# Optimization experiments

Hardware: AMD Instinct MI355X
Metric: run time of the kernel (lower is better)

## Reference

```python
import jax, jax.numpy as jnp
import numpy as np

SCALE = 1.0  # alpha / rank = 32 / 32


def setup_inputs() -> dict:
    key = jax.random.key(0)
    k_x, k_w, k_b, k_a, k_bb = jax.random.split(key, 5)
    B, S, D = 4, 4096, 3072
    depth, rank = 4, 32
    x = jax.random.normal(k_x, (B, S, D), dtype=jnp.float32)
    W = jax.random.normal(k_w, (D, D), dtype=jnp.float32) * (1.0 / np.sqrt(D))
    b = jax.random.normal(k_b, (D,), dtype=jnp.float32) * 0.02
    lora_A = jax.random.normal(k_a, (depth, rank, D), dtype=jnp.float32) * (1.0 / np.sqrt(D))
    lora_B = jax.random.normal(k_bb, (depth, D, rank), dtype=jnp.float32) * 0.02
    return {"x": x, "W": W, "b": b, "lora_A": lora_A, "lora_B": lora_B}


def reference(x, W, b, lora_A, lora_B):
    # base: y = x @ W.T + b
    base_out = jnp.einsum('bsi,oi->bso', x, W) + b
    # stacked LoRA: sum_d (x @ A_d.T @ B_d.T); dropout=0 -> identity
    # down-project to rank per depth: [B,S,depth,rank]
    z = jnp.einsum('bsi,dri->bsdr', x, lora_A)
    lora_out = jnp.einsum('bsdr,dor->bso', z, lora_B)
    return base_out + lora_out * SCALE
```

## Files before the change

kernel.cpp:

```cpp
#include <hip/hip_runtime.h>
#include <hip/hip_bf16.h>


typedef unsigned short ushort_t;
typedef short bf16x8 __attribute__((ext_vector_type(8)));
typedef float floatx4 __attribute__((ext_vector_type(4)));
typedef unsigned short ushortx4 __attribute__((ext_vector_type(4)));

__device__ __forceinline__ ushort_t f2bf(float f) {
    __hip_bfloat16 h = __float2bfloat16(f);
    return *(ushort_t*)&h;
}

__device__ __forceinline__ void async_load16(const void* g, void* l) {
    __builtin_amdgcn_global_load_lds(
        (const __attribute__((address_space(1))) void*)g,
        (__attribute__((address_space(3))) void*)l,
        16, 0, 0);
}

__global__ __launch_bounds__(256)
void cvt_kernel(const float* __restrict__ in, ushort_t* __restrict__ out, int n4) {
    int i = blockIdx.x * 256 + threadIdx.x;
    if (i < n4) {
        const float4 v = ((const float4*)in)[i];
        ushortx4 o = { f2bf(v.x), f2bf(v.y), f2bf(v.z), f2bf(v.w) };
        ((ushortx4*)out)[i] = o;
    }
}

__global__ __launch_bounds__(256)
void transpose_loraB_kernel(const float* __restrict__ lb,
                            ushort_t* __restrict__ out) {
    int idx = blockIdx.x * 256 + threadIdx.x;
    int n = idx >> 7;
    int j = idx & 127;
    int d = j >> 5, r = j & 31;
    out[idx] = f2bf(lb[(size_t)d * (3072 * 32) + (size_t)n * 32 + r]);
}

__global__ __launch_bounds__(256)
void transpose_loraA_kernel(const float* __restrict__ la,
                            ushort_t* __restrict__ out) {
    int idx = blockIdx.x * 256 + threadIdx.x;
    int kk = idx >> 7;
    int j  = idx & 127;
    out[idx] = f2bf(la[(size_t)j * 3072 + kk]);
}

template <int KT, bool OUT_F32, bool ADD_MAT>
__global__ __launch_bounds__(256)
void gemm_bt_kernel(const ushort_t* __restrict__ A, int lda,
                    const ushort_t* __restrict__ B, int ldb,
                    const float* __restrict__ Cadd,
                    const float* __restrict__ bias,
                    void* __restrict__ Cv, int ldc)
{
    __shared__ ushort_t As[128 * 32];
    __shared__ ushort_t Bs[128 * 32];

    const int t    = threadIdx.x;
    const int lane = t & 63;
    const int wave = t >> 6;
    const int wr   = wave >> 1, wc = wave & 1;
    const int quad = lane >> 4, l16 = lane & 15;

    const int mBase = blockIdx.y * 128;
    const int nBase = blockIdx.x * 128;

    floatx4 acc[4][4] = {};

    const int p0 = t,       r0 = p0 >> 2, g0 = ((p0 & 3) ^ ((r0 >> 1) & 3)) << 3;
    const int p1 = t + 256, r1 = p1 >> 2, g1 = ((p1 & 3) ^ ((r1 >> 1) & 3)) << 3;

    const int qs = (quad ^ ((l16 >> 1) & 3)) << 3;

    for (int kt = 0; kt < KT; ++kt) {
        const int ko = kt * 32;

        async_load16(A + (size_t)(mBase + r0) * lda + ko + g0, &As[p0 * 8]);
        async_load16(A + (size_t)(mBase + r1) * lda + ko + g1, &As[p1 * 8]);
        async_load16(B + (size_t)(nBase + r0) * ldb + ko + g0, &Bs[p0 * 8]);
        async_load16(B + (size_t)(nBase + r1) * ldb + ko + g1, &Bs[p1 * 8]);

        __syncthreads();

        bf16x8 af[4], bf[4];
#pragma unroll
        for (int mi = 0; mi < 4; ++mi)
            af[mi] = *(const bf16x8*)&As[(wr * 64 + mi * 16 + l16) * 32 + qs];
#pragma unroll
        for (int ni = 0; ni < 4; ++ni)
            bf[ni] = *(const bf16x8*)&Bs[(wc * 64 + ni * 16 + l16) * 32 + qs];

#pragma unroll
        for (int mi = 0; mi < 4; ++mi)
#pragma unroll
            for (int ni = 0; ni < 4; ++ni)
                acc[mi][ni] = __builtin_amdgcn_mfma_f32_16x16x32_bf16(
                    af[mi], bf[ni], acc[mi][ni], 0, 0, 0);

        __syncthreads();
    }

#pragma unroll
    for (int ni = 0; ni < 4; ++ni) {
        const int col = nBase + wc * 64 + ni * 16 + l16;
        const float bv = bias ? bias[col] : 0.0f;
#pragma unroll
        for (int mi = 0; mi < 4; ++mi) {
            const int row = mBase + wr * 64 + mi * 16 + quad * 4;
#pragma unroll
            for (int r = 0; r < 4; ++r) {
                float v = acc[mi][ni][r] + bv;
                if (ADD_MAT) v += Cadd[(size_t)(row + r) * ldc + col];
                if (OUT_F32) {
                    ((float*)Cv)[(size_t)(row + r) * ldc + col] = v;
                } else {
                    ((ushort_t*)Cv)[(size_t)(row + r) * ldc + col] = f2bf(v);
                }
            }
        }
    }
}

extern "C" void kernel_launch(void* const* d_in, const int* in_sizes, int n_in,
                              void* d_out, int out_size, void* d_ws, size_t ws_size,
                              hipStream_t stream) {
    const float* x  = (const float*)d_in[0];
    const float* W  = (const float*)d_in[1];
    const float* b  = (const float*)d_in[2];
    const float* lA = (const float*)d_in[3];
    const float* lB = (const float*)d_in[4];
    float* out = (float*)d_out;

    constexpr int M = 4 * 4096;
    constexpr int N = 3072;
    constexpr int K = 3072;
    constexpr size_t nX  = (size_t)M * K;
    constexpr size_t nW  = (size_t)N * K;
    constexpr size_t nT  = (size_t)128 * K;

    ushort_t* xb    = (ushort_t*)d_ws;
    ushort_t* Weffb = xb + nX;
    ushort_t* Bp    = Weffb + nW;
    ushort_t* At    = Bp + nT;

    cvt_kernel<<<nX / 4 / 256, 256, 0, stream>>>(x, xb, (int)(nX / 4));

    transpose_loraB_kernel<<<nT / 256, 256, 0, stream>>>(lB, Bp);
    transpose_loraA_kernel<<<nT / 256, 256, 0, stream>>>(lA, At);

    gemm_bt_kernel<4, false, true><<<dim3(N / 128, N / 128), 256, 0, stream>>>(
        Bp, 128, At, 128, W, nullptr, Weffb, N);

    gemm_bt_kernel<96, true, false><<<dim3(N / 128, M / 128), 256, 0, stream>>>(
        xb, K, Weffb, K, nullptr, b, out, N);
}
```

Before: 728.8 us.

## Replace main GEMM with 256x256 double-buffered pipelined MFMA kernel

Replaces the 128x128, single-buffered main GEMM with a 256x256-tile kernel using 512 threads, 64-wide K steps, and double-buffered LDS. Global-to-LDS async loads are interleaved with four MFMA phases per iteration, and a block-index swizzle groups neighbouring tiles for L2 reuse. The goal is to hide load latency, raise arithmetic intensity and cut barrier stalls. In exchange it uses 128KB of LDS, so only one block fits per CU, and it relies on hand-placed waitcnt and barrier ordering.

After: 636.6 us. 12.6% less time.

```diff
diff --git a/kernel.cpp b/kernel.cpp
--- a/kernel.cpp
+++ b/kernel.cpp
@@ -18,6 +18,8 @@
         (__attribute__((address_space(3))) void*)l,
         16, 0, 0);
 }
+
+#define MFMA16(a, b, c) __builtin_amdgcn_mfma_f32_16x16x32_bf16(a, b, c, 0, 0, 0)
 
 __global__ __launch_bounds__(256)
 void cvt_kernel(const float* __restrict__ in, ushort_t* __restrict__ out, int n4) {
@@ -72,7 +74,6 @@
 
     const int p0 = t,       r0 = p0 >> 2, g0 = ((p0 & 3) ^ ((r0 >> 1) & 3)) << 3;
     const int p1 = t + 256, r1 = p1 >> 2, g1 = ((p1 & 3) ^ ((r1 >> 1) & 3)) << 3;
-
     const int qs = (quad ^ ((l16 >> 1) & 3)) << 3;
 
     for (int kt = 0; kt < KT; ++kt) {
@@ -97,8 +98,7 @@
         for (int mi = 0; mi < 4; ++mi)
 #pragma unroll
             for (int ni = 0; ni < 4; ++ni)
-                acc[mi][ni] = __builtin_amdgcn_mfma_f32_16x16x32_bf16(
-                    af[mi], bf[ni], acc[mi][ni], 0, 0, 0);
+                acc[mi][ni] = MFMA16(af[mi], bf[ni], acc[mi][ni]);
 
         __syncthreads();
     }
@@ -124,6 +124,178 @@
     }
 }
 
+__global__ __launch_bounds__(512)
+void gemm256_kernel(const ushort_t* __restrict__ A,
+                    const ushort_t* __restrict__ B,
+                    const float* __restrict__ bias,
+                    float* __restrict__ C)
+{
+    constexpr int LDA = 3072;
+    constexpr int NT  = 48;
+    constexpr int NBX = 12;
+
+    __shared__ ushort_t smem_u[65536];
+    char* const smem = (char*)smem_u;
+
+    const int t    = threadIdx.x;
+    const int lane = t & 63;
+    const int wave = t >> 6;
+    const int wr   = wave >> 2;
+    const int wc   = wave & 3;
+    const int quad = lane >> 4;
+    const int l16  = lane & 15;
+
+    const int bid = blockIdx.x;
+    const int sw  = (bid & 7) * 96 + (bid >> 3);
+    const int bx  = sw % NBX;
+    const int by  = sw / NBX;
+    const int mBase = by * 256;
+    const int nBase = bx * 256;
+
+    const int prow = t >> 3;
+    const int cg   = (t & 7) ^ (prow & 7);
+    const ushort_t* const aSrc = A + (size_t)(mBase + prow) * LDA + cg * 8;
+    const ushort_t* const bSrc = B + (size_t)(nBase + prow) * LDA + cg * 8;
+    char* const aDst = smem + t * 16;
+    char* const bDst = smem + 32768 + t * 16;
+
+#define STAGE_A(c, h, kt) do {                                              \
+        const ushort_t* _s = aSrc + (size_t)(h) * 128 * LDA + (kt) * 64;    \
+        char* _d = aDst + (c) * 65536 + (h) * 16384;                        \
+        async_load16(_s, _d);                                               \
+        async_load16(_s + 64 * LDA, _d + 8192);                             \
+    } while (0)
+#define STAGE_B(c, h, kt) do {                                              \
+        const ushort_t* _s = bSrc + (size_t)(h) * 128 * LDA + (kt) * 64;    \
+        char* _d = bDst + (c) * 65536 + (h) * 16384;                        \
+        async_load16(_s, _d);                                               \
+        async_load16(_s + 64 * LDA, _d + 8192);                             \
+    } while (0)
+
+    const int s0  = ((0 + quad) ^ (l16 & 7)) << 4;
+    const int s1  = ((4 + quad) ^ (l16 & 7)) << 4;
+    const int aRd = wr * 16384 + l16 * 128;
+    const int bRd = 32768 + (wc >> 1) * 16384 + ((wc & 1) * 64 + l16) * 128;
+
+    floatx4 acc[8][4] = {};
+    bf16x8 af[8][2];
+    bf16x8 bfr[2][2];
+
+    STAGE_A(0, 0, 0); STAGE_A(0, 1, 0);
+    STAGE_B(0, 0, 0); STAGE_B(0, 1, 0);
+    STAGE_A(1, 0, 1); STAGE_A(1, 1, 1);
+    asm volatile("s_waitcnt vmcnt(4)" ::: "memory");
+    __builtin_amdgcn_s_barrier();
+    __builtin_amdgcn_sched_barrier(0);
+
+    int cur = 0;
+    for (int kt = 0; kt < NT; ++kt) {
+        const int cb  = cur << 16;
+        const int ktB = (kt + 1 < NT) ? kt + 1 : NT - 1;
+        const int ktA = (kt + 2 < NT) ? kt + 2 : NT - 1;
+
+#pragma unroll
+        for (int mi = 0; mi < 4; ++mi) {
+            af[mi][0] = *(const bf16x8*)(smem + cb + aRd + mi * 2048 + s0);
+            af[mi][1] = *(const bf16x8*)(smem + cb + aRd + mi * 2048 + s1);
+        }
+#pragma unroll
+        for (int nj = 0; nj < 2; ++nj) {
+            bfr[nj][0] = *(const bf16x8*)(smem + cb + bRd + nj * 2048 + s0);
+            bfr[nj][1] = *(const bf16x8*)(smem + cb + bRd + nj * 2048 + s1);
+        }
+        STAGE_B(cur ^ 1, 0, ktB);
+        __builtin_amdgcn_s_barrier();
+        asm volatile("s_waitcnt lgkmcnt(0)" ::: "memory");
+        __builtin_amdgcn_sched_barrier(0);
+        __builtin_amdgcn_s_setprio(1);
+#pragma unroll
+        for (int ks = 0; ks < 2; ++ks)
+#pragma unroll
+            for (int mi = 0; mi < 4; ++mi)
+#pragma unroll
+                for (int nj = 0; nj < 2; ++nj)
+                    acc[mi][nj] = MFMA16(af[mi][ks], bfr[nj][ks], acc[mi][nj]);
+        __builtin_amdgcn_s_setprio(0);
+        __builtin_amdgcn_s_barrier();
+
+#pragma unroll
+        for (int mi = 4; mi < 8; ++mi) {
+            af[mi][0] = *(const bf16x8*)(smem + cb + aRd + mi * 2048 + s0);
+            af[mi][1] = *(const bf16x8*)(smem + cb + aRd + mi * 2048 + s1);
+        }
+        STAGE_B(cur ^ 1, 1, ktB);
+        __builtin_amdgcn_s_barrier();
+        asm volatile("s_waitcnt lgkmcnt(0)" ::: "memory");
+        __builtin_amdgcn_sched_barrier(0);
+        __builtin_amdgcn_s_setprio(1);
+#pragma unroll
+        for (int ks = 0; ks < 2; ++ks)
+#pragma unroll
+            for (int mi = 4; mi < 8; ++mi)
+#pragma unroll
+                for (int nj = 0; nj < 2; ++nj)
+                    acc[mi][nj] = MFMA16(af[mi][ks], bfr[nj][ks], acc[mi][nj]);
+        __builtin_amdgcn_s_setprio(0);
+        __builtin_amdgcn_s_barrier();
+
+#pragma unroll
+        for (int nj = 0; nj < 2; ++nj) {
+            bfr[nj][0] = *(const bf16x8*)(smem + cb + bRd + (2 + nj) * 2048 + s0);
+            bfr[nj][1] = *(const bf16x8*)(smem + cb + bRd + (2 + nj) * 2048 + s1);
+        }
+        STAGE_A(cur, 0, ktA);
+        __builtin_amdgcn_s_barrier();
+        asm volatile("s_waitcnt lgkmcnt(0)" ::: "memory");
+        __builtin_amdgcn_sched_barrier(0);
+        __builtin_amdgcn_s_setprio(1);
+#pragma unroll
+        for (int ks = 0; ks < 2; ++ks)
+#pragma unroll
+            for (int mi = 0; mi < 4; ++mi)
+#pragma unroll
+                for (int nj = 0; nj < 2; ++nj)
+                    acc[mi][2 + nj] = MFMA16(af[mi][ks], bfr[nj][ks], acc[mi][2 + nj]);
+        __builtin_amdgcn_s_setprio(0);
+        __builtin_amdgcn_s_barrier();
+
+        STAGE_A(cur, 1, ktA);
+        asm volatile("s_waitcnt vmcnt(4)" ::: "memory");
+        __builtin_amdgcn_s_barrier();
+        __builtin_amdgcn_sched_barrier(0);
+        __builtin_amdgcn_s_setprio(1);
+#pragma unroll
+        for (int ks = 0; ks < 2; ++ks)
+#pragma unroll
+            for (int mi = 4; mi < 8; ++mi)
+#pragma unroll
+                for (int nj = 0; nj < 2; ++nj)
+                    acc[mi][2 + nj] = MFMA16(af[mi][ks], bfr[nj][ks], acc[mi][2 + nj]);
+        __builtin_amdgcn_s_setprio(0);
+        __builtin_amdgcn_s_barrier();
+
+        cur ^= 1;
+    }
+
+    asm volatile("s_waitcnt vmcnt(0)" ::: "memory");
+
+#pragma unroll
+    for (int ni = 0; ni < 4; ++ni) {
+        const int col = nBase + wc * 64 + ni * 16 + l16;
+        const float bv = bias[col];
+#pragma unroll
+        for (int mi = 0; mi < 8; ++mi) {
+            const int row0 = mBase + wr * 128 + mi * 16 + quad * 4;
+            float* cp = C + (size_t)row0 * LDA + col;
+#pragma unroll
+            for (int r = 0; r < 4; ++r)
+                cp[(size_t)r * LDA] = acc[mi][ni][r] + bv;
+        }
+    }
+#undef STAGE_A
+#undef STAGE_B
+}
+
 extern "C" void kernel_launch(void* const* d_in, const int* in_sizes, int n_in,
                               void* d_out, int out_size, void* d_ws, size_t ws_size,
                               hipStream_t stream) {
@@ -154,6 +326,5 @@
     gemm_bt_kernel<4, false, true><<<dim3(N / 128, N / 128), 256, 0, stream>>>(
         Bp, 128, At, 128, W, nullptr, Weffb, N);
 
-    gemm_bt_kernel<96, true, false><<<dim3(N / 128, M / 128), 256, 0, stream>>>(
-        xb, K, Weffb, K, nullptr, b, out, N);
-}
+    gemm256_kernel<<<(M / 256) * (N / 256), 512, 0, stream>>>(xb, Weffb, b, out);
+}
```
